# Optimization experiments

Hardware: AMD Instinct MI355X
Metric: run time of the kernel (lower is better)

The kernel has to match this reference:

```python
import jax, jax.numpy as jnp
import numpy as np

N_INST = 128
N_NOTES = 88
B = 64
TIME_LEN = 201
FREQ_LEN = 52
F_AFTER = (TIME_LEN - 4) * (FREQ_LEN - 4)  # 197*48 = 9456


def setup_inputs() -> dict:
    key = jax.random.key(0)
    k = jax.random.split(key, 8)
    data = jax.random.normal(k[0], (B, 1, TIME_LEN, FREQ_LEN), dtype=jnp.float32)
    w1 = jax.random.normal(k[1], (N_INST, 1, 3, 3), dtype=jnp.float32) * 0.1
    b1 = jax.random.normal(k[2], (N_INST,), dtype=jnp.float32) * 0.1
    # grouped conv: out=N_INST, in_per_group=1 (groups=N_INST)
    w2 = jax.random.normal(k[3], (N_INST, 1, 3, 3), dtype=jnp.float32) * 0.1
    b2 = jax.random.normal(k[4], (N_INST,), dtype=jnp.float32) * 0.1
    # stacked per-instrument Linear weights: [I, n_notes, F]
    wfc = jax.random.normal(k[5], (N_INST, N_NOTES, F_AFTER), dtype=jnp.float32) * 0.01
    bfc = jax.random.normal(k[6], (N_INST, N_NOTES), dtype=jnp.float32) * 0.01
    return {"data": data, "w1": w1, "b1": b1, "w2": w2, "b2": b2, "wfc": wfc, "bfc": bfc}


def reference(data, w1, b1, w2, b2, wfc, bfc):
    dn = ("NCHW", "OIHW", "NCHW")
    # conv1: 1 -> I channels, VALID 3x3
    x = jax.lax.conv_general_dilated(data, w1, (1, 1), "VALID", dimension_numbers=dn)
    x = jax.nn.relu(x + b1[None, :, None, None])
    # conv2: depthwise (groups = I), VALID 3x3
    x = jax.lax.conv_general_dilated(x, w2, (1, 1), "VALID", dimension_numbers=dn,
                                     feature_group_count=N_INST)
    x = jax.nn.relu(x + b2[None, :, None, None])
    bsz = x.shape[0]
    x = x.reshape(bsz, N_INST, -1)  # [B, I, F]
    # per-instrument Linear, batched as a single einsum (replaces the python loop)
    out = jnp.einsum("bif,inf->bin", x, wfc) + bfc[None]
    return jax.nn.sigmoid(out)
```

## Files before the change

kernel.cpp:

```cpp
#include <hip/hip_runtime.h>
#include <stdint.h>


namespace {
constexpr int kB = 64, kI = 128, kN = 88, kT = 201, kF = 52;
constexpr int kT2 = 197, kF2 = 48;
constexpr int kFTOT = kT2 * kF2;
constexpr int kTHREADS = 384;
constexpr int kOUT = kB * kI * kN;
constexpr int kNP = 96;
constexpr int kLDB2 = 104;
constexpr int kNCH = 12;
constexpr int kNH = 44;
constexpr int kLDK = 200;
constexpr int kSLABS = 50;

typedef float f32x4 __attribute__((ext_vector_type(4)));
typedef __bf16 bf16x8 __attribute__((ext_vector_type(8)));
typedef unsigned short u16x8 __attribute__((ext_vector_type(8)));
typedef unsigned short u16x4 __attribute__((ext_vector_type(4)));

#define BAR_LGKM() asm volatile("s_waitcnt lgkmcnt(0)\n\ts_barrier" ::: "memory")

__device__ __forceinline__ unsigned short bf16_rne(float f) {
  unsigned int u = __float_as_uint(f);
  u += 0x7fffu + ((u >> 16) & 1u);
  return (unsigned short)(u >> 16);
}

__device__ __forceinline__ void loadrow(float* d, const float* p) {
  float4 a = *(const float4*)p;
  float4 b = *(const float4*)(p + 4);
  float4 c = *(const float4*)(p + 8);
  d[0] = a.x; d[1] = a.y; d[2] = a.z;  d[3] = a.w;
  d[4] = b.x; d[5] = b.y; d[6] = b.z;  d[7] = b.w;
  d[8] = c.x; d[9] = c.y; d[10] = c.z; d[11] = c.w;
}

__device__ __forceinline__ void c1row(float* o, const float* r0, const float* r1,
                                      const float* r2, const float* w, float bias) {
#pragma unroll
  for (int c = 0; c < 10; ++c) {
    float v = bias;
    v += r0[c] * w[0]; v += r0[c + 1] * w[1]; v += r0[c + 2] * w[2];
    v += r1[c] * w[3]; v += r1[c + 1] * w[4]; v += r1[c + 2] * w[5];
    v += r2[c] * w[6]; v += r2[c + 1] * w[7]; v += r2[c + 2] * w[8];
    o[c] = fmaxf(v, 0.0f);
  }
}

__device__ __forceinline__ u16x8 conv2row(const float* cx, const float* cy,
                                          const float* cz, const float* w2r,
                                          float b2r) {
  u16x8 o8;
#pragma unroll
  for (int c = 0; c < 8; ++c) {
    float v = b2r;
    v += cx[c] * w2r[0] + cx[c + 1] * w2r[1] + cx[c + 2] * w2r[2];
    v += cy[c] * w2r[3] + cy[c + 1] * w2r[4] + cy[c + 2] * w2r[5];
    v += cz[c] * w2r[6] + cz[c + 1] * w2r[7] + cz[c + 2] * w2r[8];
    o8[c] = bf16_rne(fmaxf(v, 0.0f));
  }
  return o8;
}
}

__global__ __launch_bounds__(kTHREADS, 2) void fused2_kernel(
    const float* __restrict__ data, const float* __restrict__ w1,
    const float* __restrict__ b1, const float* __restrict__ w2,
    const float* __restrict__ b2, const float* __restrict__ wfc,
    float* __restrict__ partial) {
  __shared__ unsigned short As[2][kNCH * 64 * 8];
  __shared__ unsigned short Bs[2][kNP * kLDB2];
  const int tid = threadIdx.x;
  const int i = blockIdx.x >> 1, kh = blockIdx.x & 1;
  const int r0 = kh ? 98 : 0;
  const int nslab = kh ? 50 : 49;

  for (int z = tid; z < 8 * kLDB2; z += kTHREADS) {
    Bs[0][kN * kLDB2 + z] = 0;
    Bs[1][kN * kLDB2 + z] = 0;
  }

  const int bb = tid / 6, oc = tid - bb * 6;
  const float* dbase = data + bb * (kT * kF) + oc * 8;
  float w1r[9], w2r[9];
#pragma unroll
  for (int j = 0; j < 9; ++j) { w1r[j] = w1[i * 9 + j]; w2r[j] = w2[i * 9 + j]; }
  const float b1r = b1[i], b2r = b2[i];

  const float* wbase = wfc + (size_t)i * kN * kFTOT;
  float4 W[6];
  auto loadW = [&](int s) {
    const int kbase = (r0 + 2 * s) * kF2;
#pragma unroll
    for (int j = 0; j < 6; ++j) {
      int q = tid + kTHREADS * j;
      if (q < kN * 24) {
        int n = q / 24, k4 = q - n * 24;
        int kg = kbase + k4 * 4;
        if (kg + 4 <= kFTOT) {
          W[j] = *(const float4*)(wbase + (size_t)n * kFTOT + kg);
        } else {
          W[j] = make_float4(0.f, 0.f, 0.f, 0.f);
        }
      }
    }
  };
  loadW(0);

  const int wv = tid >> 6, ln = tid & 63;
  const int lc = ln & 15, lq = ln >> 4;
  f32x4 acc[4];
#pragma unroll
  for (int mt = 0; mt < 4; ++mt) acc[mt] = (f32x4){0.f, 0.f, 0.f, 0.f};

  for (int s = 0; s < nslab; ++s) {
    const int p = s & 1;
#pragma unroll
    for (int j = 0; j < 6; ++j) {
      int q = tid + kTHREADS * j;
      if (q < kN * 24) {
        int n = q / 24, k4 = q - n * 24;
        u16x4 o;
        o[0] = bf16_rne(W[j].x); o[1] = bf16_rne(W[j].y);
        o[2] = bf16_rne(W[j].z); o[3] = bf16_rne(W[j].w);
        *(u16x4*)(&Bs[p][n * kLDB2 + k4 * 4]) = o;
      }
    }
    {
      const int t0 = r0 + 2 * s;
      const bool row1ok = (t0 + 1) < kT2;
      float d0[12], d1[12], d2[12], d3[12], d4[12], d5[12];
      float c0[10], c1v[10], c2[10], c3[10];
      loadrow(d0, dbase + (t0 + 0) * kF);
      loadrow(d1, dbase + (t0 + 1) * kF);
      loadrow(d2, dbase + (t0 + 2) * kF);
      loadrow(d3, dbase + (t0 + 3) * kF);
      loadrow(d4, dbase + (t0 + 4) * kF);
      if (row1ok) loadrow(d5, dbase + (t0 + 5) * kF);
      c1row(c0, d0, d1, d2, w1r, b1r);
      c1row(c1v, d1, d2, d3, w1r, b1r);
      c1row(c2, d2, d3, d4, w1r, b1r);
      u16x8 oA = conv2row(c0, c1v, c2, w2r, b2r);
      u16x8 oB;
      if (row1ok) {
        c1row(c3, d3, d4, d5, w1r, b1r);
        oB = conv2row(c1v, c2, c3, w2r, b2r);
      } else {
        u16x8 z = {0, 0, 0, 0, 0, 0, 0, 0};
        oB = z;
      }
      const int cA = oc, cB = 6 + oc;
      *(u16x8*)(&As[p][(cA * 64 + ((bb + cA) & 63)) * 8]) = oA;
      *(u16x8*)(&As[p][(cB * 64 + ((bb + cB) & 63)) * 8]) = oB;
    }
    loadW(s + 1);
    BAR_LGKM();
    const unsigned short* Ap = As[p];
    const unsigned short* Bp = &Bs[p][(wv * 16 + lc) * kLDB2 + lq * 8];
#pragma unroll
    for (int ks = 0; ks < 3; ++ks) {
      bf16x8 bfrag = *(const bf16x8*)(Bp + ks * 32);
      const int c = ks * 4 + lq;
#pragma unroll
      for (int mt = 0; mt < 4; ++mt) {
        const int m = mt * 16 + lc;
        bf16x8 afrag = *(const bf16x8*)(Ap + (c * 64 + ((m + c) & 63)) * 8);
        acc[mt] = __builtin_amdgcn_mfma_f32_16x16x32_bf16(afrag, bfrag, acc[mt], 0, 0, 0);
      }
    }
  }

  float* dst = partial + (size_t)kh * kOUT;
  const int n = wv * 16 + lc;
  if (n < kN) {
#pragma unroll
    for (int mt = 0; mt < 4; ++mt) {
#pragma unroll
      for (int r = 0; r < 4; ++r) {
        const int b = mt * 16 + lq * 4 + r;
        dst[(size_t)(b * kI + i) * kN + n] = acc[mt][r];
      }
    }
  }
}

__global__ __launch_bounds__(256) void reduce_sigmoid_kernel(
    const float* __restrict__ partial, const float* __restrict__ bfc,
    float* __restrict__ out) {
  const int idx = blockIdx.x * 256 + threadIdx.x;
  if (idx >= kOUT) return;
  const int n = idx % kN;
  const int i = (idx / kN) % kI;
  const float v = partial[idx] + partial[kOUT + idx] + bfc[i * kN + n];
  out[idx] = 1.0f / (1.0f + __expf(-v));
}

__global__ __launch_bounds__(kTHREADS, 2) void fused_conv_fc_kernel(
    const float* __restrict__ data, const float* __restrict__ w1,
    const float* __restrict__ b1, const float* __restrict__ w2,
    const float* __restrict__ b2, const float* __restrict__ wfc,
    const float* __restrict__ bfc, float* __restrict__ out) {
  __shared__ unsigned short Ab[kB * kLDK];
  __shared__ unsigned short Bb[48 * kLDK];
  const int tid = threadIdx.x;
  const int i = blockIdx.x >> 1;
  const int nh = blockIdx.x & 1;
  const int nbase = nh * kNH;
  for (int z = tid; z < 4 * kLDK; z += kTHREADS) Bb[kNH * kLDK + z] = 0;
  float w1r[9], w2r[9];
#pragma unroll
  for (int j = 0; j < 9; ++j) { w1r[j] = w1[i * 9 + j]; w2r[j] = w2[i * 9 + j]; }
  const float b1r = b1[i], b2r = b2[i];
  const int bb = tid / 6;
  const int oc = tid - bb * 6;
  const int fr0 = oc * 8;
  const float* dbase = data + bb * (kT * kF) + fr0;
  float c1[6][10];
  float dA[12], dB[12], dC[12], dD[12];
  float4 W[6];
  loadrow(dC, dbase + 0 * kF);
  loadrow(dD, dbase + 1 * kF);
  loadrow(dA, dbase + 2 * kF);
  loadrow(dB, dbase + 3 * kF);
  c1row(c1[0], dC, dD, dA, w1r, b1r);
  c1row(c1[1], dD, dA, dB, w1r, b1r);
#pragma unroll
  for (int j = 0; j < 6; ++j) {
    int q = tid + kTHREADS * j;
    if (q < kNH * 48) {
      int n = q / 48, k4 = q - n * 48;
      W[j] = *(const float4*)(wfc + (size_t)(i * kN + nbase + n) * kFTOT + k4 * 4);
    } else {
      W[j] = make_float4(0.f, 0.f, 0.f, 0.f);
    }
  }
  const int wv = tid >> 6, ln = tid & 63;
  const int nt = wv % 3, mp = wv / 3;
  const int lc = ln & 15, lq = ln >> 4;
  f32x4 acc0 = {0.f, 0.f, 0.f, 0.f};
  f32x4 acc1 = {0.f, 0.f, 0.f, 0.f};
  for (int s = 0; s < kSLABS; ++s) {
    loadrow(dC, dbase + (4 * s + 4) * kF);
    c1row(c1[2], dA, dB, dC, w1r, b1r);
    if (s < kSLABS - 1) {
      loadrow(dD, dbase + (4 * s + 5) * kF);
      c1row(c1[3], dB, dC, dD, w1r, b1r);
      loadrow(dA, dbase + (4 * s + 6) * kF);
      c1row(c1[4], dC, dD, dA, w1r, b1r);
      loadrow(dB, dbase + (4 * s + 7) * kF);
      c1row(c1[5], dD, dA, dB, w1r, b1r);
    }
#pragma unroll
    for (int tl = 0; tl < 4; ++tl) {
      if (tl == 0 || s < kSLABS - 1) {
        u16x8 o8;
#pragma unroll
        for (int c = 0; c < 8; ++c) {
          float v = b2r;
#pragma unroll
          for (int r = 0; r < 3; ++r) {
            v += c1[tl + r][c] * w2r[3 * r];
            v += c1[tl + r][c + 1] * w2r[3 * r + 1];
            v += c1[tl + r][c + 2] * w2r[3 * r + 2];
          }
          o8[c] = bf16_rne(fmaxf(v, 0.0f));
        }
        *(u16x8*)&Ab[bb * kLDK + tl * 48 + fr0] = o8;
      }
    }
#pragma unroll
    for (int j = 0; j < 6; ++j) {
      int q = tid + kTHREADS * j;
      if (q < kNH * 48) {
        int n = q / 48, k4 = q - n * 48;
        u16x4 o;
        o[0] = bf16_rne(W[j].x); o[1] = bf16_rne(W[j].y);
        o[2] = bf16_rne(W[j].z); o[3] = bf16_rne(W[j].w);
        *(u16x4*)&Bb[n * kLDK + k4 * 4] = o;
      }
    }
    if (s + 1 < kSLABS) {
      const int real4 = (s + 1 == kSLABS - 1) ? 12 : 48;
#pragma unroll
      for (int j = 0; j < 6; ++j) {
        int q = tid + kTHREADS * j;
        int n = q / 48, k4 = q - n * 48;
        if (q < kNH * 48 && k4 < real4) {
          W[j] = *(const float4*)(wfc + (size_t)(i * kN + nbase + n) * kFTOT +
                                  (size_t)(s + 1) * 192 + k4 * 4);
        } else {
          W[j] = make_float4(0.f, 0.f, 0.f, 0.f);
        }
      }
    }
    __syncthreads();
    {
      const unsigned short* Ar0 = &Ab[(mp * 32 + lc) * kLDK];
      const unsigned short* Ar1 = Ar0 + 16 * kLDK;
      const unsigned short* Br = &Bb[(nt * 16 + lc) * kLDK];
      const int kq = lq * 8;
      const int kmax = (s != kSLABS - 1) ? 6 : 2;
      for (int ks = 0; ks < kmax; ++ks) {
        int ko = ks * 32 + kq;
        bf16x8 a0 = *(const bf16x8*)(Ar0 + ko);
        bf16x8 a1 = *(const bf16x8*)(Ar1 + ko);
        bf16x8 bfr = *(const bf16x8*)(Br + ko);
        acc0 = __builtin_amdgcn_mfma_f32_16x16x32_bf16(a0, bfr, acc0, 0, 0, 0);
        acc1 = __builtin_amdgcn_mfma_f32_16x16x32_bf16(a1, bfr, acc1, 0, 0, 0);
      }
    }
    __syncthreads();
    if (s < kSLABS - 1) {
#pragma unroll
      for (int c = 0; c < 10; ++c) { c1[0][c] = c1[4][c]; c1[1][c] = c1[5][c]; }
    }
  }
  const int nl = nt * 16 + lc;
  if (nl < kNH) {
    const int ng = nbase + nl;
    const float bias = bfc[i * kN + ng];
#pragma unroll
    for (int r = 0; r < 4; ++r) {
      int b0 = mp * 32 + lq * 4 + r;
      float v0 = acc0[r] + bias;
      out[(size_t)(b0 * kI + i) * kN + ng] = 1.0f / (1.0f + __expf(-v0));
      float v1 = acc1[r] + bias;
      out[(size_t)((b0 + 16) * kI + i) * kN + ng] = 1.0f / (1.0f + __expf(-v1));
    }
  }
}

extern "C" void kernel_launch(void* const* d_in, const int* in_sizes, int n_in,
                              void* d_out, int out_size, void* d_ws, size_t ws_size,
                              hipStream_t stream) {
  const float* data = (const float*)d_in[0];
  const float* w1 = (const float*)d_in[1];
  const float* b1 = (const float*)d_in[2];
  const float* w2 = (const float*)d_in[3];
  const float* b2 = (const float*)d_in[4];
  const float* wfc = (const float*)d_in[5];
  const float* bfc = (const float*)d_in[6];
  float* out = (float*)d_out;
  const size_t pb = (size_t)kOUT * 4;
  if (ws_size >= 2 * pb) {
    float* part = (float*)d_ws;
    fused2_kernel<<<dim3(kI * 2), dim3(kTHREADS), 0, stream>>>(
        data, w1, b1, w2, b2, wfc, part);
    reduce_sigmoid_kernel<<<dim3((kOUT + 255) / 256), dim3(256), 0, stream>>>(
        part, bfc, out);
  } else {
    fused_conv_fc_kernel<<<dim3(kI * 2), dim3(kTHREADS), 0, stream>>>(
        data, w1, b1, w2, b2, wfc, bfc, out);
  }
}
```

Before: 708.0 us.

## Split K across four groups per instrument and reuse conv1 rows across slabs

Splits the reduction dimension into four chunks per instrument instead of two, launching 512 blocks, and raises the launch-bounds occupancy hint to three blocks. The reduce kernel now sums four partial buffers. Conv1 output rows are carried across slab iterations in registers, so each slab loads four input rows instead of six and computes two conv1 rows instead of four. The last weight prefetch is also skipped. The cost is more partial-buffer traffic in the reduce step, and higher register pressure under the tighter launch bound could cause spills.

```diff
diff --git a/kernel.cpp b/kernel.cpp
--- a/kernel.cpp
+++ b/kernel.cpp
@@ -11,6 +11,7 @@
 constexpr int kNP = 96;
 constexpr int kLDB2 = 104;
 constexpr int kNCH = 12;
+constexpr int kNG = 4;
 constexpr int kNH = 44;
 constexpr int kLDK = 200;
 constexpr int kSLABS = 50;
@@ -65,7 +66,7 @@
 }
 }
 
-__global__ __launch_bounds__(kTHREADS, 2) void fused2_kernel(
+__global__ __launch_bounds__(kTHREADS, 3) void fused2_kernel(
     const float* __restrict__ data, const float* __restrict__ w1,
     const float* __restrict__ b1, const float* __restrict__ w2,
     const float* __restrict__ b2, const float* __restrict__ wfc,
@@ -73,9 +74,9 @@
   __shared__ unsigned short As[2][kNCH * 64 * 8];
   __shared__ unsigned short Bs[2][kNP * kLDB2];
   const int tid = threadIdx.x;
-  const int i = blockIdx.x >> 1, kh = blockIdx.x & 1;
-  const int r0 = kh ? 98 : 0;
-  const int nslab = kh ? 50 : 49;
+  const int i = blockIdx.x >> 2, g = blockIdx.x & 3;
+  const int r0 = g * 50;
+  const int nslab = (g == 3) ? 24 : 25;
 
   for (int z = tid; z < 8 * kLDB2; z += kTHREADS) {
     Bs[0][kN * kLDB2 + z] = 0;
@@ -109,6 +110,17 @@
   };
   loadW(0);
 
+  float cc0[10], cc1[10];
+  {
+    float dp0[12], dp1[12], dp2[12], dp3[12];
+    loadrow(dp0, dbase + (r0 + 0) * kF);
+    loadrow(dp1, dbase + (r0 + 1) * kF);
+    loadrow(dp2, dbase + (r0 + 2) * kF);
+    loadrow(dp3, dbase + (r0 + 3) * kF);
+    c1row(cc0, dp0, dp1, dp2, w1r, b1r);
+    c1row(cc1, dp1, dp2, dp3, w1r, b1r);
+  }
+
   const int wv = tid >> 6, ln = tid & 63;
   const int lc = ln & 15, lq = ln >> 4;
   f32x4 acc[4];
@@ -131,22 +143,18 @@
     {
       const int t0 = r0 + 2 * s;
       const bool row1ok = (t0 + 1) < kT2;
-      float d0[12], d1[12], d2[12], d3[12], d4[12], d5[12];
-      float c0[10], c1v[10], c2[10], c3[10];
-      loadrow(d0, dbase + (t0 + 0) * kF);
-      loadrow(d1, dbase + (t0 + 1) * kF);
-      loadrow(d2, dbase + (t0 + 2) * kF);
-      loadrow(d3, dbase + (t0 + 3) * kF);
-      loadrow(d4, dbase + (t0 + 4) * kF);
-      if (row1ok) loadrow(d5, dbase + (t0 + 5) * kF);
-      c1row(c0, d0, d1, d2, w1r, b1r);
-      c1row(c1v, d1, d2, d3, w1r, b1r);
-      c1row(c2, d2, d3, d4, w1r, b1r);
-      u16x8 oA = conv2row(c0, c1v, c2, w2r, b2r);
+      float d2r[12], d3r[12], d4r[12], d5r[12];
+      float c2[10], c3[10];
+      loadrow(d2r, dbase + (t0 + 2) * kF);
+      loadrow(d3r, dbase + (t0 + 3) * kF);
+      loadrow(d4r, dbase + (t0 + 4) * kF);
+      if (row1ok) loadrow(d5r, dbase + (t0 + 5) * kF);
+      c1row(c2, d2r, d3r, d4r, w1r, b1r);
+      u16x8 oA = conv2row(cc0, cc1, c2, w2r, b2r);
       u16x8 oB;
       if (row1ok) {
-        c1row(c3, d3, d4, d5, w1r, b1r);
-        oB = conv2row(c1v, c2, c3, w2r, b2r);
+        c1row(c3, d3r, d4r, d5r, w1r, b1r);
+        oB = conv2row(cc1, c2, c3, w2r, b2r);
       } else {
         u16x8 z = {0, 0, 0, 0, 0, 0, 0, 0};
         oB = z;
@@ -154,8 +162,10 @@
       const int cA = oc, cB = 6 + oc;
       *(u16x8*)(&As[p][(cA * 64 + ((bb + cA) & 63)) * 8]) = oA;
       *(u16x8*)(&As[p][(cB * 64 + ((bb + cB) & 63)) * 8]) = oB;
-    }
-    loadW(s + 1);
+#pragma unroll
+      for (int c = 0; c < 10; ++c) { cc0[c] = c2[c]; cc1[c] = c3[c]; }
+    }
+    if (s + 1 < nslab) loadW(s + 1);
     BAR_LGKM();
     const unsigned short* Ap = As[p];
     const unsigned short* Bp = &Bs[p][(wv * 16 + lc) * kLDB2 + lq * 8];
@@ -172,7 +182,7 @@
     }
   }
 
-  float* dst = partial + (size_t)kh * kOUT;
+  float* dst = partial + (size_t)g * kOUT;
   const int n = wv * 16 + lc;
   if (n < kN) {
 #pragma unroll
@@ -193,7 +203,8 @@
   if (idx >= kOUT) return;
   const int n = idx % kN;
   const int i = (idx / kN) % kI;
-  const float v = partial[idx] + partial[kOUT + idx] + bfc[i * kN + n];
+  const float v = partial[idx] + partial[kOUT + idx] + partial[2 * kOUT + idx] +
+                  partial[3 * kOUT + idx] + bfc[i * kN + n];
   out[idx] = 1.0f / (1.0f + __expf(-v));
 }
 
@@ -344,9 +355,9 @@
   const float* bfc = (const float*)d_in[6];
   float* out = (float*)d_out;
   const size_t pb = (size_t)kOUT * 4;
-  if (ws_size >= 2 * pb) {
+  if (ws_size >= kNG * pb) {
     float* part = (float*)d_ws;
-    fused2_kernel<<<dim3(kI * 2), dim3(kTHREADS), 0, stream>>>(
+    fused2_kernel<<<dim3(kI * kNG), dim3(kTHREADS), 0, stream>>>(
         data, w1, b1, w2, b2, wfc, part);
     reduce_sigmoid_kernel<<<dim3((kOUT + 255) / 256), dim3(256), 0, stream>>>(
         part, bfc, out);
```

Result: slower. 815.6 us (+15.2%).

## Split K into four groups and load FC weights directly into MFMA registers

Applied to the files above, without the earlier changes.

The fused conv+FC kernel now splits the reduction dimension into four row groups per instrument instead of two, so it launches 512 blocks instead of 256 and allows three blocks per CU. The weight tile is no longer staged through shared memory. Each lane loads its own B-fragment from global memory straight into registers and converts it to bf16 before the MFMA, which removes the Bs buffer, its LDS writes and the software prefetch. The trade-offs are twice as much partial-sum traffic in the reduce kernel, more scattered global loads of weights, and no longer overlapping the weight loads with the previous slab's compute.

```diff
diff --git a/kernel.cpp b/kernel.cpp
--- a/kernel.cpp
+++ b/kernel.cpp
@@ -8,9 +8,8 @@
 constexpr int kFTOT = kT2 * kF2;
 constexpr int kTHREADS = 384;
 constexpr int kOUT = kB * kI * kN;
-constexpr int kNP = 96;
-constexpr int kLDB2 = 104;
 constexpr int kNCH = 12;
+constexpr int kNG = 4;
 constexpr int kNH = 44;
 constexpr int kLDK = 200;
 constexpr int kSLABS = 50;
@@ -65,22 +64,16 @@
 }
 }
 
-__global__ __launch_bounds__(kTHREADS, 2) void fused2_kernel(
+__global__ __launch_bounds__(kTHREADS, 3) void fused3_kernel(
     const float* __restrict__ data, const float* __restrict__ w1,
     const float* __restrict__ b1, const float* __restrict__ w2,
     const float* __restrict__ b2, const float* __restrict__ wfc,
     float* __restrict__ partial) {
   __shared__ unsigned short As[2][kNCH * 64 * 8];
-  __shared__ unsigned short Bs[2][kNP * kLDB2];
   const int tid = threadIdx.x;
-  const int i = blockIdx.x >> 1, kh = blockIdx.x & 1;
-  const int r0 = kh ? 98 : 0;
-  const int nslab = kh ? 50 : 49;
-
-  for (int z = tid; z < 8 * kLDB2; z += kTHREADS) {
-    Bs[0][kN * kLDB2 + z] = 0;
-    Bs[1][kN * kLDB2 + z] = 0;
-  }
+  const int i = blockIdx.x >> 2, g = blockIdx.x & 3;
+  const int r0 = g * 50;
+  const int nslab = (g == 3) ? 24 : 25;
 
   const int bb = tid / 6, oc = tid - bb * 6;
   const float* dbase = data + bb * (kT * kF) + oc * 8;
@@ -89,56 +82,45 @@
   for (int j = 0; j < 9; ++j) { w1r[j] = w1[i * 9 + j]; w2r[j] = w2[i * 9 + j]; }
   const float b1r = b1[i], b2r = b2[i];
 
-  const float* wbase = wfc + (size_t)i * kN * kFTOT;
-  float4 W[6];
-  auto loadW = [&](int s) {
-    const int kbase = (r0 + 2 * s) * kF2;
-#pragma unroll
-    for (int j = 0; j < 6; ++j) {
-      int q = tid + kTHREADS * j;
-      if (q < kN * 24) {
-        int n = q / 24, k4 = q - n * 24;
-        int kg = kbase + k4 * 4;
-        if (kg + 4 <= kFTOT) {
-          W[j] = *(const float4*)(wbase + (size_t)n * kFTOT + kg);
-        } else {
-          W[j] = make_float4(0.f, 0.f, 0.f, 0.f);
-        }
-      }
-    }
-  };
-  loadW(0);
-
   const int wv = tid >> 6, ln = tid & 63;
   const int lc = ln & 15, lq = ln >> 4;
+  const int nB = wv * 16 + lc;
+  const bool nOK = (nB < kN);
+  const float* wrow = wfc + ((size_t)i * kN + (nOK ? nB : 0)) * kFTOT;
+
   f32x4 acc[4];
 #pragma unroll
   for (int mt = 0; mt < 4; ++mt) acc[mt] = (f32x4){0.f, 0.f, 0.f, 0.f};
 
   for (int s = 0; s < nslab; ++s) {
     const int p = s & 1;
-#pragma unroll
-    for (int j = 0; j < 6; ++j) {
-      int q = tid + kTHREADS * j;
-      if (q < kN * 24) {
-        int n = q / 24, k4 = q - n * 24;
-        u16x4 o;
-        o[0] = bf16_rne(W[j].x); o[1] = bf16_rne(W[j].y);
-        o[2] = bf16_rne(W[j].z); o[3] = bf16_rne(W[j].w);
-        *(u16x4*)(&Bs[p][n * kLDB2 + k4 * 4]) = o;
-      }
-    }
+    const int t0 = r0 + 2 * s;
+    const bool row1ok = (t0 + 1) < kT2;
+
+    float d0[12], d1[12], d2[12], d3[12], d4[12], d5[12];
+    loadrow(d0, dbase + (t0 + 0) * kF);
+    loadrow(d1, dbase + (t0 + 1) * kF);
+    loadrow(d2, dbase + (t0 + 2) * kF);
+    loadrow(d3, dbase + (t0 + 3) * kF);
+    loadrow(d4, dbase + (t0 + 4) * kF);
+    if (row1ok) loadrow(d5, dbase + (t0 + 5) * kF);
+
+    const int kb0 = t0 * kF2 + lq * 8;
+    float4 bfr[6];
+#pragma unroll
+    for (int ks = 0; ks < 3; ++ks) {
+      const int kk = kb0 + ks * 32;
+      if (nOK && kk + 8 <= kFTOT) {
+        bfr[2 * ks]     = *(const float4*)(wrow + kk);
+        bfr[2 * ks + 1] = *(const float4*)(wrow + kk + 4);
+      } else {
+        bfr[2 * ks]     = make_float4(0.f, 0.f, 0.f, 0.f);
+        bfr[2 * ks + 1] = make_float4(0.f, 0.f, 0.f, 0.f);
+      }
+    }
+
     {
-      const int t0 = r0 + 2 * s;
-      const bool row1ok = (t0 + 1) < kT2;
-      float d0[12], d1[12], d2[12], d3[12], d4[12], d5[12];
       float c0[10], c1v[10], c2[10], c3[10];
-      loadrow(d0, dbase + (t0 + 0) * kF);
-      loadrow(d1, dbase + (t0 + 1) * kF);
-      loadrow(d2, dbase + (t0 + 2) * kF);
-      loadrow(d3, dbase + (t0 + 3) * kF);
-      loadrow(d4, dbase + (t0 + 4) * kF);
-      if (row1ok) loadrow(d5, dbase + (t0 + 5) * kF);
       c1row(c0, d0, d1, d2, w1r, b1r);
       c1row(c1v, d1, d2, d3, w1r, b1r);
       c1row(c2, d2, d3, d4, w1r, b1r);
@@ -155,13 +137,17 @@
       *(u16x8*)(&As[p][(cA * 64 + ((bb + cA) & 63)) * 8]) = oA;
       *(u16x8*)(&As[p][(cB * 64 + ((bb + cB) & 63)) * 8]) = oB;
     }
-    loadW(s + 1);
     BAR_LGKM();
+
     const unsigned short* Ap = As[p];
-    const unsigned short* Bp = &Bs[p][(wv * 16 + lc) * kLDB2 + lq * 8];
 #pragma unroll
     for (int ks = 0; ks < 3; ++ks) {
-      bf16x8 bfrag = *(const bf16x8*)(Bp + ks * 32);
+      u16x8 t;
+      t[0] = bf16_rne(bfr[2 * ks].x);     t[1] = bf16_rne(bfr[2 * ks].y);
+      t[2] = bf16_rne(bfr[2 * ks].z);     t[3] = bf16_rne(bfr[2 * ks].w);
+      t[4] = bf16_rne(bfr[2 * ks + 1].x); t[5] = bf16_rne(bfr[2 * ks + 1].y);
+      t[6] = bf16_rne(bfr[2 * ks + 1].z); t[7] = bf16_rne(bfr[2 * ks + 1].w);
+      bf16x8 bfrag = *(bf16x8*)&t;
       const int c = ks * 4 + lq;
 #pragma unroll
       for (int mt = 0; mt < 4; ++mt) {
@@ -172,15 +158,14 @@
     }
   }
 
-  float* dst = partial + (size_t)kh * kOUT;
-  const int n = wv * 16 + lc;
-  if (n < kN) {
+  float* dst = partial + (size_t)g * kOUT;
+  if (nOK) {
 #pragma unroll
     for (int mt = 0; mt < 4; ++mt) {
 #pragma unroll
       for (int r = 0; r < 4; ++r) {
         const int b = mt * 16 + lq * 4 + r;
-        dst[(size_t)(b * kI + i) * kN + n] = acc[mt][r];
+        dst[(size_t)(b * kI + i) * kN + nB] = acc[mt][r];
       }
     }
   }
@@ -193,7 +178,8 @@
   if (idx >= kOUT) return;
   const int n = idx % kN;
   const int i = (idx / kN) % kI;
-  const float v = partial[idx] + partial[kOUT + idx] + bfc[i * kN + n];
+  const float v = partial[idx] + partial[kOUT + idx] + partial[2 * kOUT + idx] +
+                  partial[3 * kOUT + idx] + bfc[i * kN + n];
   out[idx] = 1.0f / (1.0f + __expf(-v));
 }
 
@@ -344,9 +330,9 @@
   const float* bfc = (const float*)d_in[6];
   float* out = (float*)d_out;
   const size_t pb = (size_t)kOUT * 4;
-  if (ws_size >= 2 * pb) {
+  if (ws_size >= kNG * pb) {
     float* part = (float*)d_ws;
-    fused2_kernel<<<dim3(kI * 2), dim3(kTHREADS), 0, stream>>>(
+    fused3_kernel<<<dim3(kI * kNG), dim3(kTHREADS), 0, stream>>>(
         data, w1, b1, w2, b2, wfc, part);
     reduce_sigmoid_kernel<<<dim3((kOUT + 255) / 256), dim3(256), 0, stream>>>(
         part, bfc, out);
```

Result: slower. 860.6 us (+21.5%).
